# Performance work log

Hardware: AMD Instinct MI355X
Metric: run time of the kernel (lower is better)

The kernel has to match this reference:

```python
import jax, jax.numpy as jnp
import numpy as np

N = 100000      # nodes
E = 1600000     # edges (avg degree 16)
D_IN, D_H, D_OUT = 128, 128, 64
EPS = 1e-5      # BatchNorm1d eps


def setup_inputs() -> dict:
    key = jax.random.key(0)
    ks = jax.random.split(key, 8)
    x = jax.random.normal(ks[0], (N, D_IN), jnp.float32)
    edge_index = jax.random.randint(ks[1], (2, E), 0, N, dtype=jnp.int64)

    def glorot(k, i, o):
        return jax.random.normal(k, (i, o), jnp.float32) * np.float32(1.0 / np.sqrt(i))

    return {
        "x": x,
        "edge_index": edge_index,
        "W1": glorot(ks[2], D_IN, D_H), "b1": jnp.zeros((D_H,), jnp.float32),
        "g1": jnp.ones((D_H,), jnp.float32), "be1": jnp.zeros((D_H,), jnp.float32),
        "W2": glorot(ks[3], D_H, D_H), "b2": jnp.zeros((D_H,), jnp.float32),
        "g2": jnp.ones((D_H,), jnp.float32), "be2": jnp.zeros((D_H,), jnp.float32),
        "W3": glorot(ks[4], D_H, D_OUT), "b3": jnp.zeros((D_OUT,), jnp.float32),
    }


def gcn_conv(h, W, b, src, dst, norm_e, self_norm):
    # GCNConv: D^{-1/2}(A+I)D^{-1/2} h W + b  (self-loops handled analytically)
    hw = h @ W                                  # [N, out]
    msg = hw[src] * norm_e[:, None]             # [E, out] gather + scale
    agg = jax.ops.segment_sum(msg, dst, num_segments=N)
    return agg + hw * self_norm[:, None] + b


def batchnorm(x, g, b):
    mu = jnp.mean(x, axis=0)
    var = jnp.var(x, axis=0)
    return (x - mu) * jax.lax.rsqrt(var + EPS) * g + b


def reference(x, edge_index, W1, b1, g1, be1, W2, b2, g2, be2, W3, b3):
    src, dst = edge_index[0], edge_index[1]
    # degrees including self-loop
    deg = jax.ops.segment_sum(jnp.ones((E,), jnp.float32), dst, num_segments=N) + 1.0
    dis = jax.lax.rsqrt(deg)                    # deg^{-1/2}
    norm_e = dis[src] * dis[dst]                # per-edge norm
    self_norm = dis * dis                       # self-loop norm deg^{-1}

    h = jax.nn.relu(batchnorm(gcn_conv(x, W1, b1, src, dst, norm_e, self_norm), g1, be1))
    h = jax.nn.relu(batchnorm(gcn_conv(h, W2, b2, src, dst, norm_e, self_norm), g2, be2))
    return gcn_conv(h, W3, b3, src, dst, norm_e, self_norm)
```

## Files before the change

kernel.cpp:

```cpp
#include <hip/hip_runtime.h>
#include <hip/hip_bf16.h>

#define BN_EPS 1e-5f
#define BINSH 9
#define MAXNB 200
#define NBLK 256

typedef __attribute__((ext_vector_type(8))) short bf16x8v;
typedef __attribute__((ext_vector_type(4))) float f32x4v;

__device__ __forceinline__ float u2f(unsigned x) { return __uint_as_float(x); }
__device__ __forceinline__ unsigned short f2bf(float f) {
    union { __hip_bfloat16 h; unsigned short u; } cv;
    cv.h = __float2bfloat16(f);
    return cv.u;
}

__global__ void detect_kernel(const int* __restrict__ e32, int* __restrict__ flag) {
    if (threadIdx.x == 0 && blockIdx.x == 0) {
        int nz = 0;
        for (int i = 0; i < 64; ++i) nz += (e32[2*i + 1] != 0);
        *flag = (nz == 0) ? 1 : 0;
    }
}

__device__ __forceinline__ int edge_at(const void* p, long long i, int is64) {
    return is64 ? (int)((const long long*)p)[i] : ((const int*)p)[i];
}

__global__ __launch_bounds__(256) void histA_kernel(const void* __restrict__ eidx,
                                                    const int* __restrict__ flag,
                                                    int* __restrict__ hist2dT,
                                                    int* __restrict__ binhist,
                                                    int E, int NB, int per_block) {
    __shared__ int lh[MAXNB];
    const int t = threadIdx.x;
    for (int i = t; i < NB; i += 256) lh[i] = 0;
    __syncthreads();
    const int is64 = *flag;
    long long base = (long long)blockIdx.x * per_block;
    long long lim  = base + per_block;
    if (lim > E) lim = E;
    for (long long e = base + t; e < lim; e += 256) {
        int d = edge_at(eidx, (long long)E + e, is64);
        atomicAdd(&lh[d >> BINSH], 1);
    }
    __syncthreads();
    for (int i = t; i < NB; i += 256) {
        hist2dT[i * NBLK + blockIdx.x] = lh[i];
        atomicAdd(&binhist[i], lh[i]);
    }
}

__global__ void binscan_kernel(const int* __restrict__ binhist, int* __restrict__ binrp, int NB) {
    __shared__ int s[256];
    const int t = threadIdx.x;
    int v = (t < NB) ? binhist[t] : 0;
    s[t] = v;
    __syncthreads();
    for (int off = 1; off < 256; off <<= 1) {
        int x = (t >= off) ? s[t - off] : 0;
        __syncthreads();
        s[t] += x;
        __syncthreads();
    }
    if (t < NB) binrp[t] = s[t] - v;
    if (t == 0) binrp[NB] = s[255];
}

__global__ __launch_bounds__(256) void colscan_kernel(int* __restrict__ hist2dT,
                                                      const int* __restrict__ binrp) {
    __shared__ int s[256];
    const int b = blockIdx.x;
    const int t = threadIdx.x;
    int v = hist2dT[b * NBLK + t];
    s[t] = v;
    __syncthreads();
    for (int off = 1; off < 256; off <<= 1) {
        int x = (t >= off) ? s[t - off] : 0;
        __syncthreads();
        s[t] += x;
        __syncthreads();
    }
    hist2dT[b * NBLK + t] = binrp[b] + s[t] - v;
}

__global__ __launch_bounds__(256) void passB_kernel(const void* __restrict__ eidx,
                                                    const int* __restrict__ flag,
                                                    const int* __restrict__ hist2dT,
                                                    int2* __restrict__ ibuf,
                                                    int E, int NB, int per_block) {
    __shared__ int lbase[MAXNB];
    __shared__ int lcur[MAXNB];
    const int t = threadIdx.x;
    for (int i = t; i < NB; i += 256) {
        lbase[i] = hist2dT[i * NBLK + blockIdx.x];
        lcur[i]  = 0;
    }
    __syncthreads();
    const int is64 = *flag;
    long long base = (long long)blockIdx.x * per_block;
    long long lim  = base + per_block;
    if (lim > E) lim = E;
    for (long long e = base + t; e < lim; e += 256) {
        int sN = edge_at(eidx, e, is64);
        int d  = edge_at(eidx, (long long)E + e, is64);
        int b  = d >> BINSH;
        int pos = lbase[b] + atomicAdd(&lcur[b], 1);
        ibuf[pos] = make_int2(sN, d);
    }
}

__global__ __launch_bounds__(256) void binsort2_kernel(const int2* __restrict__ ibuf,
                                                       const int* __restrict__ binrp,
                                                       int* __restrict__ rp,
                                                       float* __restrict__ dis,
                                                       int2* __restrict__ ep, int N) {
    const int b  = blockIdx.x;
    const int d0 = b << BINSH;
    const int dc = min(1 << BINSH, N - d0);
    __shared__ int lcnt[1 << BINSH];
    __shared__ int lofs[1 << BINSH];
    __shared__ int s2[256];
    const int t = threadIdx.x;
    lcnt[t] = 0; lcnt[t + 256] = 0;
    __syncthreads();
    const int ib0 = binrp[b], ib1 = binrp[b + 1];
    const int nE  = ib1 - ib0;
    for (int i = t; i < nE; i += 256) {
        int2 sd = ibuf[ib0 + i];
        atomicAdd(&lcnt[sd.y - d0], 1);
    }
    __syncthreads();
    const int c0 = lcnt[2 * t], c1 = lcnt[2 * t + 1];
    const int pair = c0 + c1;
    s2[t] = pair;
    __syncthreads();
    for (int off = 1; off < 256; off <<= 1) {
        int x = (t >= off) ? s2[t - off] : 0;
        __syncthreads();
        s2[t] += x;
        __syncthreads();
    }
    const int pexcl = s2[t] - pair;
    if (2 * t < dc) {
        rp[d0 + 2 * t + 1] = ib0 + pexcl + c0;
        dis[d0 + 2 * t]    = rsqrtf((float)c0 + 1.0f);
    }
    if (2 * t + 1 < dc) {
        rp[d0 + 2 * t + 2] = ib0 + pexcl + pair;
        dis[d0 + 2 * t + 1] = rsqrtf((float)c1 + 1.0f);
    }
    if (b == 0 && t == 0) rp[0] = 0;
    lofs[2 * t]     = pexcl;
    lofs[2 * t + 1] = pexcl + c0;
    __syncthreads();
    for (int i = t; i < nE; i += 256) {
        int2 sd = ibuf[ib0 + i];
        int dl  = sd.y - d0;
        int pos = ib0 + atomicAdd(&lofs[dl], 1);
        ep[pos] = sd;
    }
}

__global__ void weight_kernel(int2* __restrict__ ep, const float* __restrict__ dis, int E) {
    int e = blockIdx.x * 256 + threadIdx.x;
    if (e >= E) return;
    int2 sd = ep[e];
    float w = dis[sd.x] * dis[sd.y];
    ep[e] = make_int2(sd.x, __float_as_int(w));
}

__global__ void prep_wt_kernel(const float* __restrict__ W, __hip_bfloat16* __restrict__ Wt,
                               int K, int DOUT) {
    int i = blockIdx.x * 256 + threadIdx.x;
    if (i < K * DOUT) {
        int k = i / DOUT, c = i % DOUT;
        Wt[c * K + k] = __float2bfloat16(W[i]);
    }
}

__device__ __forceinline__ void load8(const float* p, float* f) {
    float4 v0 = ((const float4*)p)[0];
    float4 v1 = ((const float4*)p)[1];
    f[0] = v0.x; f[1] = v0.y; f[2] = v0.z; f[3] = v0.w;
    f[4] = v1.x; f[5] = v1.y; f[6] = v1.z; f[7] = v1.w;
}
__device__ __forceinline__ void load8(const __hip_bfloat16* p, float* f) {
    uint4 v = *(const uint4*)p;
    f[0] = u2f(v.x << 16); f[1] = u2f(v.x & 0xffff0000u);
    f[2] = u2f(v.y << 16); f[3] = u2f(v.y & 0xffff0000u);
    f[4] = u2f(v.z << 16); f[5] = u2f(v.z & 0xffff0000u);
    f[6] = u2f(v.w << 16); f[7] = u2f(v.w & 0xffff0000u);
}

template <int DOUT, bool BN, typename TH>
__global__ __launch_bounds__(256) void mfma_gemm_kernel(const TH* __restrict__ H,
                                                        const __hip_bfloat16* __restrict__ Wt,
                                                        const float* __restrict__ bnst,
                                                        __hip_bfloat16* __restrict__ out, int N) {
    constexpr int NCT = DOUT / 16;
    constexpr int LDW = 136;
    __shared__ __hip_bfloat16 sWt[DOUT * LDW];
    const int t = threadIdx.x;
    for (int i = t; i < DOUT * 16; i += 256) {
        int row = i >> 4, seg = i & 15;
        *(uint4*)&sWt[row * LDW + seg * 8] = ((const uint4*)Wt)[i];
    }
    const int lane = t & 63, wid = t >> 6;
    const int kq = lane >> 4, mrow = lane & 15;
    const int grow = blockIdx.x * 64 + wid * 16 + mrow;
    const int lrow = min(grow, N - 1);
    bf16x8v afrag[4];
#pragma unroll
    for (int ks = 0; ks < 4; ++ks) {
        const int k0 = ks * 32 + kq * 8;
        float f[8];
        load8(H + (size_t)lrow * 128 + k0, f);
        if (BN) {
            float4 s0 = *(const float4*)(bnst + k0);
            float4 s1 = *(const float4*)(bnst + k0 + 4);
            float4 h0 = *(const float4*)(bnst + 128 + k0);
            float4 h1 = *(const float4*)(bnst + 128 + k0 + 4);
            f[0] = fmaxf(fmaf(f[0], s0.x, h0.x), 0.f);
            f[1] = fmaxf(fmaf(f[1], s0.y, h0.y), 0.f);
            f[2] = fmaxf(fmaf(f[2], s0.z, h0.z), 0.f);
            f[3] = fmaxf(fmaf(f[3], s0.w, h0.w), 0.f);
            f[4] = fmaxf(fmaf(f[4], s1.x, h1.x), 0.f);
            f[5] = fmaxf(fmaf(f[5], s1.y, h1.y), 0.f);
            f[6] = fmaxf(fmaf(f[6], s1.z, h1.z), 0.f);
            f[7] = fmaxf(fmaf(f[7], s1.w, h1.w), 0.f);
        }
        bf16x8v a;
#pragma unroll
        for (int j = 0; j < 8; ++j) a[j] = (short)f2bf(f[j]);
        afrag[ks] = a;
    }
    __syncthreads();
    f32x4v acc[NCT];
#pragma unroll
    for (int ct = 0; ct < NCT; ++ct) acc[ct] = (f32x4v){0.f, 0.f, 0.f, 0.f};
#pragma unroll
    for (int ct = 0; ct < NCT; ++ct) {
#pragma unroll
        for (int ks = 0; ks < 4; ++ks) {
            bf16x8v b = *(const bf16x8v*)&sWt[(ct * 16 + mrow) * LDW + ks * 32 + kq * 8];
            acc[ct] = __builtin_amdgcn_mfma_f32_16x16x32_bf16(afrag[ks], b, acc[ct], 0, 0, 0);
        }
    }
#pragma unroll
    for (int r = 0; r < 4; ++r) {
        int orow = blockIdx.x * 64 + wid * 16 + kq * 4 + r;
        if (orow < N) {
            __hip_bfloat16* op = out + (size_t)orow * DOUT + mrow;
#pragma unroll
            for (int ct = 0; ct < NCT; ++ct) {
                union { unsigned short u; __hip_bfloat16 h; } cv;
                cv.u = f2bf(acc[ct][r]);
                op[ct * 16] = cv.h;
            }
        }
    }
}

template <int D, bool OUTBF>
__global__ void agg_kernel(const __hip_bfloat16* __restrict__ hw, const int* __restrict__ rp,
                           const int2* __restrict__ ep, const float* __restrict__ dis,
                           const float* __restrict__ bias, void* __restrict__ outv, int N) {
    constexpr int LPR = D / 4;
    int gtid = blockIdx.x * blockDim.x + threadIdx.x;
    int n    = gtid / LPR;
    int lane = gtid % LPR;
    if (n >= N) return;
    const uint2* hw4 = (const uint2*)hw;
    float sn = dis[n];
    sn *= sn;
    uint2 hv = hw4[(size_t)n * LPR + lane];
    float a0 = u2f(hv.x << 16) * sn;
    float a1 = u2f(hv.x & 0xffff0000u) * sn;
    float a2 = u2f(hv.y << 16) * sn;
    float a3 = u2f(hv.y & 0xffff0000u) * sn;
    int e0 = rp[n], e1 = rp[n + 1];
    int e = e0;
    for (; e + 8 <= e1; e += 8) {
        int2 p[8];
        uint2 v[8];
#pragma unroll
        for (int j = 0; j < 8; ++j) p[j] = ep[e + j];
#pragma unroll
        for (int j = 0; j < 8; ++j) v[j] = hw4[(size_t)p[j].x * LPR + lane];
#pragma unroll
        for (int j = 0; j < 8; ++j) {
            float w = __int_as_float(p[j].y);
            a0 += u2f(v[j].x << 16) * w; a1 += u2f(v[j].x & 0xffff0000u) * w;
            a2 += u2f(v[j].y << 16) * w; a3 += u2f(v[j].y & 0xffff0000u) * w;
        }
    }
    for (; e + 4 <= e1; e += 4) {
        int2 p[4];
        uint2 v[4];
#pragma unroll
        for (int j = 0; j < 4; ++j) p[j] = ep[e + j];
#pragma unroll
        for (int j = 0; j < 4; ++j) v[j] = hw4[(size_t)p[j].x * LPR + lane];
#pragma unroll
        for (int j = 0; j < 4; ++j) {
            float w = __int_as_float(p[j].y);
            a0 += u2f(v[j].x << 16) * w; a1 += u2f(v[j].x & 0xffff0000u) * w;
            a2 += u2f(v[j].y << 16) * w; a3 += u2f(v[j].y & 0xffff0000u) * w;
        }
    }
    for (; e < e1; ++e) {
        int2 p = ep[e];
        uint2 v = hw4[(size_t)p.x * LPR + lane];
        float w = __int_as_float(p.y);
        a0 += u2f(v.x << 16) * w; a1 += u2f(v.x & 0xffff0000u) * w;
        a2 += u2f(v.y << 16) * w; a3 += u2f(v.y & 0xffff0000u) * w;
    }
    float4 bv = ((const float4*)bias)[lane];
    a0 += bv.x; a1 += bv.y; a2 += bv.z; a3 += bv.w;
    if (OUTBF) {
        ushort4 o;
        o.x = f2bf(a0); o.y = f2bf(a1); o.z = f2bf(a2); o.w = f2bf(a3);
        ((ushort4*)outv)[(size_t)n * LPR + lane] = o;
    } else {
        ((float4*)outv)[(size_t)n * LPR + lane] = make_float4(a0, a1, a2, a3);
    }
}

__global__ void bn_stats_kernel(const __hip_bfloat16* __restrict__ X, float* __restrict__ stats, int N) {
    const int t  = threadIdx.x;
    const int c4 = t & 31;
    const int rg = t >> 5;
    const uint2* X4 = (const uint2*)X;
    float s0=0,s1=0,s2=0,s3=0,q0=0,q1=0,q2=0,q3=0;
    for (int r = blockIdx.x * 8 + rg; r < N; r += gridDim.x * 8) {
        uint2 v = X4[(size_t)r * 32 + c4];
        float f0 = u2f(v.x << 16), f1 = u2f(v.x & 0xffff0000u);
        float f2 = u2f(v.y << 16), f3 = u2f(v.y & 0xffff0000u);
        s0 += f0; q0 += f0 * f0;
        s1 += f1; q1 += f1 * f1;
        s2 += f2; q2 += f2 * f2;
        s3 += f3; q3 += f3 * f3;
    }
    __shared__ float ls[8][32][8];
    ls[rg][c4][0] = s0; ls[rg][c4][1] = s1; ls[rg][c4][2] = s2; ls[rg][c4][3] = s3;
    ls[rg][c4][4] = q0; ls[rg][c4][5] = q1; ls[rg][c4][6] = q2; ls[rg][c4][7] = q3;
    __syncthreads();
    if (t < 32) {
        float a[8] = {0,0,0,0,0,0,0,0};
        for (int g = 0; g < 8; ++g)
            for (int k = 0; k < 8; ++k) a[k] += ls[g][t][k];
        for (int k = 0; k < 4; ++k) {
            atomicAdd(&stats[t * 4 + k], a[k]);
            atomicAdd(&stats[128 + t * 4 + k], a[4 + k]);
        }
    }
}

__global__ void bn_finalize_kernel(float* __restrict__ stats, const float* __restrict__ g,
                                   const float* __restrict__ be, float invN) {
    int c = threadIdx.x;
    if (c < 128) {
        float mu  = stats[c] * invN;
        float var = stats[c + 128] * invN - mu * mu;
        float sc  = g[c] * rsqrtf(var + BN_EPS);
        stats[c]       = sc;
        stats[c + 128] = be[c] - mu * sc;
    }
}

extern "C" void kernel_launch(void* const* d_in, const int* in_sizes, int n_in,
                              void* d_out, int out_size, void* d_ws, size_t ws_size,
                              hipStream_t stream) {
    const float* x   = (const float*)d_in[0];
    const void*  eix = d_in[1];
    const float* W1  = (const float*)d_in[2];
    const float* b1  = (const float*)d_in[3];
    const float* g1  = (const float*)d_in[4];
    const float* be1 = (const float*)d_in[5];
    const float* W2  = (const float*)d_in[6];
    const float* b2  = (const float*)d_in[7];
    const float* g2  = (const float*)d_in[8];
    const float* be2 = (const float*)d_in[9];
    const float* W3  = (const float*)d_in[10];
    const float* b3  = (const float*)d_in[11];
    float* outp = (float*)d_out;

    const int N = in_sizes[0] / 128;
    const int E = in_sizes[1] / 2;
    const int NB = (N + (1 << BINSH) - 1) >> BINSH;

    char* base = (char*)d_ws;
    size_t off = 0;
    auto alloc = [&](size_t bytes) -> char* {
        char* p = base + off;
        off = (off + bytes + 255) & ~(size_t)255;
        return p;
    };
    __hip_bfloat16* A = (__hip_bfloat16*)alloc((size_t)N * 128 * 2);
    __hip_bfloat16* B = (__hip_bfloat16*)alloc((size_t)N * 128 * 2);
    int*   rp      = (int*)alloc((size_t)(N + 1) * 4);
    float* dis     = (float*)alloc((size_t)N * 4);
    int2*  ep      = (int2*)alloc((size_t)E * 8);
    int2*  ibuf    = (int2*)alloc((size_t)E * 8);
    int*   hist2dT = (int*)alloc((size_t)MAXNB * NBLK * 4);
    int*   binhist = (int*)alloc(MAXNB * 4);
    int*   binrp   = (int*)alloc((MAXNB + 1) * 4);
    __hip_bfloat16* wt1 = (__hip_bfloat16*)alloc(128 * 128 * 2);
    __hip_bfloat16* wt2 = (__hip_bfloat16*)alloc(128 * 128 * 2);
    __hip_bfloat16* wt3 = (__hip_bfloat16*)alloc(64 * 128 * 2);
    float* stats1 = (float*)alloc(256 * 4);
    float* stats2 = (float*)alloc(256 * 4);
    int*   flag   = (int*)alloc(64);
    (void)ws_size; (void)n_in; (void)out_size;

    const int per_block = (E + NBLK - 1) / NBLK;

    detect_kernel<<<1, 64, 0, stream>>>((const int*)eix, flag);
    hipMemsetAsync(binhist, 0, MAXNB * 4, stream);
    histA_kernel<<<NBLK, 256, 0, stream>>>(eix, flag, hist2dT, binhist, E, NB, per_block);
    binscan_kernel<<<1, 256, 0, stream>>>(binhist, binrp, NB);
    colscan_kernel<<<NB, 256, 0, stream>>>(hist2dT, binrp);
    passB_kernel<<<NBLK, 256, 0, stream>>>(eix, flag, hist2dT, ibuf, E, NB, per_block);
    binsort2_kernel<<<NB, 256, 0, stream>>>(ibuf, binrp, rp, dis, ep, N);
    weight_kernel<<<(E + 255) / 256, 256, 0, stream>>>(ep, dis, E);

    prep_wt_kernel<<<64, 256, 0, stream>>>(W1, wt1, 128, 128);
    prep_wt_kernel<<<64, 256, 0, stream>>>(W2, wt2, 128, 128);
    prep_wt_kernel<<<32, 256, 0, stream>>>(W3, wt3, 128, 64);

    const float invN = 1.0f / (float)N;
    const int gemm_grid = (N + 63) / 64;
    const int agg128_grid  = (int)(((long long)N * 32 + 255) / 256);
    const int agg64_grid   = (int)(((long long)N * 16 + 255) / 256);

    mfma_gemm_kernel<128, false, float><<<gemm_grid, 256, 0, stream>>>(x, wt1, nullptr, A, N);
    agg_kernel<128, true><<<agg128_grid, 256, 0, stream>>>(A, rp, ep, dis, b1, B, N);
    hipMemsetAsync(stats1, 0, 256 * 4, stream);
    bn_stats_kernel<<<256, 256, 0, stream>>>(B, stats1, N);
    bn_finalize_kernel<<<1, 128, 0, stream>>>(stats1, g1, be1, invN);

    mfma_gemm_kernel<128, true, __hip_bfloat16><<<gemm_grid, 256, 0, stream>>>(B, wt2, stats1, A, N);
    agg_kernel<128, true><<<agg128_grid, 256, 0, stream>>>(A, rp, ep, dis, b2, B, N);
    hipMemsetAsync(stats2, 0, 256 * 4, stream);
    bn_stats_kernel<<<256, 256, 0, stream>>>(B, stats2, N);
    bn_finalize_kernel<<<1, 128, 0, stream>>>(stats2, g2, be2, invN);

    mfma_gemm_kernel<64, true, __hip_bfloat16><<<gemm_grid, 256, 0, stream>>>(B, wt3, stats2, A, N);
    agg_kernel<64, false><<<agg64_grid, 256, 0, stream>>>(A, rp, ep, dis, b3, outp, N);
}
```

Measured before the change: 375.9 us.

## Fuse BN stats into aggregation, finalize into GEMM, merge small setup kernels

Batch-norm sum and sum-of-squares are now accumulated inside the aggregation kernel through shared-memory then global atomics, and the finalize step is recomputed per block inside the next GEMM. This removes the separate stats and finalize kernels and their extra pass over the hidden activations. The aggregation also moves to 8 features per lane with 16-byte gathers and 4-way unrolling instead of 8-way. Detection of the edge-index width is folded into the histogram kernels, the three weight-prep launches become one, and the memsets are merged, which cuts launch count. In exchange the code adds shared-memory atomic contention in the aggregation and one atomic flush per block to global stats.

Result: slower. 613.5 us (+63.2%).

```diff
diff --git a/kernel.cpp b/kernel.cpp
--- a/kernel.cpp
+++ b/kernel.cpp
@@ -16,28 +16,31 @@
     return cv.u;
 }
 
-__global__ void detect_kernel(const int* __restrict__ e32, int* __restrict__ flag) {
-    if (threadIdx.x == 0 && blockIdx.x == 0) {
-        int nz = 0;
-        for (int i = 0; i < 64; ++i) nz += (e32[2*i + 1] != 0);
-        *flag = (nz == 0) ? 1 : 0;
-    }
-}
-
 __device__ __forceinline__ int edge_at(const void* p, long long i, int is64) {
     return is64 ? (int)((const long long*)p)[i] : ((const int*)p)[i];
 }
 
+__device__ __forceinline__ int detect_is64(const void* eidx, int* sflag, int t) {
+    if (t == 0) {
+        const int* e32 = (const int*)eidx;
+        int nz = 0;
+        for (int i = 0; i < 64; ++i) nz += (e32[2 * i + 1] != 0);
+        *sflag = (nz == 0) ? 1 : 0;
+    }
+    return 0;
+}
+
 __global__ __launch_bounds__(256) void histA_kernel(const void* __restrict__ eidx,
-                                                    const int* __restrict__ flag,
                                                     int* __restrict__ hist2dT,
                                                     int* __restrict__ binhist,
                                                     int E, int NB, int per_block) {
     __shared__ int lh[MAXNB];
-    const int t = threadIdx.x;
+    __shared__ int sflag;
+    const int t = threadIdx.x;
+    detect_is64(eidx, &sflag, t);
     for (int i = t; i < NB; i += 256) lh[i] = 0;
     __syncthreads();
-    const int is64 = *flag;
+    const int is64 = sflag;
     long long base = (long long)blockIdx.x * per_block;
     long long lim  = base + per_block;
     if (lim > E) lim = E;
@@ -86,19 +89,20 @@
 }
 
 __global__ __launch_bounds__(256) void passB_kernel(const void* __restrict__ eidx,
-                                                    const int* __restrict__ flag,
                                                     const int* __restrict__ hist2dT,
                                                     int2* __restrict__ ibuf,
                                                     int E, int NB, int per_block) {
     __shared__ int lbase[MAXNB];
     __shared__ int lcur[MAXNB];
-    const int t = threadIdx.x;
+    __shared__ int sflag;
+    const int t = threadIdx.x;
+    detect_is64(eidx, &sflag, t);
     for (int i = t; i < NB; i += 256) {
         lbase[i] = hist2dT[i * NBLK + blockIdx.x];
         lcur[i]  = 0;
     }
     __syncthreads();
-    const int is64 = *flag;
+    const int is64 = sflag;
     long long base = (long long)blockIdx.x * per_block;
     long long lim  = base + per_block;
     if (lim > E) lim = E;
@@ -171,12 +175,23 @@
     ep[e] = make_int2(sd.x, __float_as_int(w));
 }
 
-__global__ void prep_wt_kernel(const float* __restrict__ W, __hip_bfloat16* __restrict__ Wt,
-                               int K, int DOUT) {
+__global__ void prep_wt_all_kernel(const float* __restrict__ W1, const float* __restrict__ W2,
+                                   const float* __restrict__ W3,
+                                   __hip_bfloat16* __restrict__ wt1,
+                                   __hip_bfloat16* __restrict__ wt2,
+                                   __hip_bfloat16* __restrict__ wt3) {
     int i = blockIdx.x * 256 + threadIdx.x;
-    if (i < K * DOUT) {
-        int k = i / DOUT, c = i % DOUT;
-        Wt[c * K + k] = __float2bfloat16(W[i]);
+    if (i < 16384) {
+        int k = i >> 7, c = i & 127;
+        wt1[c * 128 + k] = __float2bfloat16(W1[i]);
+    } else if (i < 32768) {
+        int j = i - 16384;
+        int k = j >> 7, c = j & 127;
+        wt2[c * 128 + k] = __float2bfloat16(W2[j]);
+    } else if (i < 40960) {
+        int j = i - 32768;
+        int k = j >> 6, c = j & 63;
+        wt3[c * 128 + k] = __float2bfloat16(W3[j]);
     }
 }
 
@@ -197,16 +212,28 @@
 template <int DOUT, bool BN, typename TH>
 __global__ __launch_bounds__(256) void mfma_gemm_kernel(const TH* __restrict__ H,
                                                         const __hip_bfloat16* __restrict__ Wt,
-                                                        const float* __restrict__ bnst,
+                                                        const float* __restrict__ stats,
+                                                        const float* __restrict__ g,
+                                                        const float* __restrict__ be,
+                                                        float invN,
                                                         __hip_bfloat16* __restrict__ out, int N) {
     constexpr int NCT = DOUT / 16;
     constexpr int LDW = 136;
     __shared__ __hip_bfloat16 sWt[DOUT * LDW];
+    __shared__ float sBN[256];
     const int t = threadIdx.x;
     for (int i = t; i < DOUT * 16; i += 256) {
         int row = i >> 4, seg = i & 15;
         *(uint4*)&sWt[row * LDW + seg * 8] = ((const uint4*)Wt)[i];
     }
+    if (BN && t < 128) {
+        float mu  = stats[t] * invN;
+        float var = stats[128 + t] * invN - mu * mu;
+        float sc  = g[t] * rsqrtf(var + BN_EPS);
+        sBN[t]       = sc;
+        sBN[128 + t] = be[t] - mu * sc;
+    }
+    __syncthreads();
     const int lane = t & 63, wid = t >> 6;
     const int kq = lane >> 4, mrow = lane & 15;
     const int grow = blockIdx.x * 64 + wid * 16 + mrow;
@@ -218,10 +245,10 @@
         float f[8];
         load8(H + (size_t)lrow * 128 + k0, f);
         if (BN) {
-            float4 s0 = *(const float4*)(bnst + k0);
-            float4 s1 = *(const float4*)(bnst + k0 + 4);
-            float4 h0 = *(const float4*)(bnst + 128 + k0);
-            float4 h1 = *(const float4*)(bnst + 128 + k0 + 4);
+            float4 s0 = *(const float4*)&sBN[k0];
+            float4 s1 = *(const float4*)&sBN[k0 + 4];
+            float4 h0 = *(const float4*)&sBN[128 + k0];
+            float4 h1 = *(const float4*)&sBN[128 + k0 + 4];
             f[0] = fmaxf(fmaf(f[0], s0.x, h0.x), 0.f);
             f[1] = fmaxf(fmaf(f[1], s0.y, h0.y), 0.f);
             f[2] = fmaxf(fmaf(f[2], s0.z, h0.z), 0.f);
@@ -236,7 +263,6 @@
         for (int j = 0; j < 8; ++j) a[j] = (short)f2bf(f[j]);
         afrag[ks] = a;
     }
-    __syncthreads();
     f32x4v acc[NCT];
 #pragma unroll
     for (int ct = 0; ct < NCT; ++ct) acc[ct] = (f32x4v){0.f, 0.f, 0.f, 0.f};
@@ -263,110 +289,93 @@
     }
 }
 
-template <int D, bool OUTBF>
-__global__ void agg_kernel(const __hip_bfloat16* __restrict__ hw, const int* __restrict__ rp,
-                           const int2* __restrict__ ep, const float* __restrict__ dis,
-                           const float* __restrict__ bias, void* __restrict__ outv, int N) {
-    constexpr int LPR = D / 4;
-    int gtid = blockIdx.x * blockDim.x + threadIdx.x;
-    int n    = gtid / LPR;
-    int lane = gtid % LPR;
-    if (n >= N) return;
-    const uint2* hw4 = (const uint2*)hw;
-    float sn = dis[n];
-    sn *= sn;
-    uint2 hv = hw4[(size_t)n * LPR + lane];
-    float a0 = u2f(hv.x << 16) * sn;
-    float a1 = u2f(hv.x & 0xffff0000u) * sn;
-    float a2 = u2f(hv.y << 16) * sn;
-    float a3 = u2f(hv.y & 0xffff0000u) * sn;
-    int e0 = rp[n], e1 = rp[n + 1];
-    int e = e0;
-    for (; e + 8 <= e1; e += 8) {
-        int2 p[8];
-        uint2 v[8];
-#pragma unroll
-        for (int j = 0; j < 8; ++j) p[j] = ep[e + j];
-#pragma unroll
-        for (int j = 0; j < 8; ++j) v[j] = hw4[(size_t)p[j].x * LPR + lane];
-#pragma unroll
-        for (int j = 0; j < 8; ++j) {
-            float w = __int_as_float(p[j].y);
-            a0 += u2f(v[j].x << 16) * w; a1 += u2f(v[j].x & 0xffff0000u) * w;
-            a2 += u2f(v[j].y << 16) * w; a3 += u2f(v[j].y & 0xffff0000u) * w;
-        }
-    }
-    for (; e + 4 <= e1; e += 4) {
-        int2 p[4];
-        uint2 v[4];
-#pragma unroll
-        for (int j = 0; j < 4; ++j) p[j] = ep[e + j];
-#pragma unroll
-        for (int j = 0; j < 4; ++j) v[j] = hw4[(size_t)p[j].x * LPR + lane];
-#pragma unroll
-        for (int j = 0; j < 4; ++j) {
-            float w = __int_as_float(p[j].y);
-            a0 += u2f(v[j].x << 16) * w; a1 += u2f(v[j].x & 0xffff0000u) * w;
-            a2 += u2f(v[j].y << 16) * w; a3 += u2f(v[j].y & 0xffff0000u) * w;
-        }
-    }
-    for (; e < e1; ++e) {
-        int2 p = ep[e];
-        uint2 v = hw4[(size_t)p.x * LPR + lane];
-        float w = __int_as_float(p.y);
-        a0 += u2f(v.x << 16) * w; a1 += u2f(v.x & 0xffff0000u) * w;
-        a2 += u2f(v.y << 16) * w; a3 += u2f(v.y & 0xffff0000u) * w;
-    }
-    float4 bv = ((const float4*)bias)[lane];
-    a0 += bv.x; a1 += bv.y; a2 += bv.z; a3 += bv.w;
-    if (OUTBF) {
-        ushort4 o;
-        o.x = f2bf(a0); o.y = f2bf(a1); o.z = f2bf(a2); o.w = f2bf(a3);
-        ((ushort4*)outv)[(size_t)n * LPR + lane] = o;
-    } else {
-        ((float4*)outv)[(size_t)n * LPR + lane] = make_float4(a0, a1, a2, a3);
-    }
-}
-
-__global__ void bn_stats_kernel(const __hip_bfloat16* __restrict__ X, float* __restrict__ stats, int N) {
-    const int t  = threadIdx.x;
-    const int c4 = t & 31;
-    const int rg = t >> 5;
-    const uint2* X4 = (const uint2*)X;
-    float s0=0,s1=0,s2=0,s3=0,q0=0,q1=0,q2=0,q3=0;
-    for (int r = blockIdx.x * 8 + rg; r < N; r += gridDim.x * 8) {
-        uint2 v = X4[(size_t)r * 32 + c4];
-        float f0 = u2f(v.x << 16), f1 = u2f(v.x & 0xffff0000u);
-        float f2 = u2f(v.y << 16), f3 = u2f(v.y & 0xffff0000u);
-        s0 += f0; q0 += f0 * f0;
-        s1 += f1; q1 += f1 * f1;
-        s2 += f2; q2 += f2 * f2;
-        s3 += f3; q3 += f3 * f3;
-    }
-    __shared__ float ls[8][32][8];
-    ls[rg][c4][0] = s0; ls[rg][c4][1] = s1; ls[rg][c4][2] = s2; ls[rg][c4][3] = s3;
-    ls[rg][c4][4] = q0; ls[rg][c4][5] = q1; ls[rg][c4][6] = q2; ls[rg][c4][7] = q3;
-    __syncthreads();
-    if (t < 32) {
-        float a[8] = {0,0,0,0,0,0,0,0};
-        for (int g = 0; g < 8; ++g)
-            for (int k = 0; k < 8; ++k) a[k] += ls[g][t][k];
-        for (int k = 0; k < 4; ++k) {
-            atomicAdd(&stats[t * 4 + k], a[k]);
-            atomicAdd(&stats[128 + t * 4 + k], a[4 + k]);
-        }
-    }
-}
-
-__global__ void bn_finalize_kernel(float* __restrict__ stats, const float* __restrict__ g,
-                                   const float* __restrict__ be, float invN) {
-    int c = threadIdx.x;
-    if (c < 128) {
-        float mu  = stats[c] * invN;
-        float var = stats[c + 128] * invN - mu * mu;
-        float sc  = g[c] * rsqrtf(var + BN_EPS);
-        stats[c]       = sc;
-        stats[c + 128] = be[c] - mu * sc;
+__device__ __forceinline__ void acc8(float* a, uint4 v, float w) {
+    a[0] += u2f(v.x << 16) * w;  a[1] += u2f(v.x & 0xffff0000u) * w;
+    a[2] += u2f(v.y << 16) * w;  a[3] += u2f(v.y & 0xffff0000u) * w;
+    a[4] += u2f(v.z << 16) * w;  a[5] += u2f(v.z & 0xffff0000u) * w;
+    a[6] += u2f(v.w << 16) * w;  a[7] += u2f(v.w & 0xffff0000u) * w;
+}
+
+template <int D, bool OUTBF, bool STATS>
+__global__ __launch_bounds__(256) void agg_kernel(const __hip_bfloat16* __restrict__ hw,
+                                                  const int* __restrict__ rp,
+                                                  const int2* __restrict__ ep,
+                                                  const float* __restrict__ dis,
+                                                  const float* __restrict__ bias,
+                                                  void* __restrict__ outv,
+                                                  float* __restrict__ stats, int N) {
+    constexpr int LPR = D / 8;
+    __shared__ float ssum[128];
+    __shared__ float ssq[128];
+    const int t = threadIdx.x;
+    if (STATS) {
+        if (t < 128) { ssum[t] = 0.f; ssq[t] = 0.f; }
+        __syncthreads();
+    }
+    const int gtid = blockIdx.x * 256 + t;
+    const int n    = gtid / LPR;
+    const int lane = gtid % LPR;
+    const bool valid = (n < N);
+    const uint4* hw8 = (const uint4*)hw;
+    float a[8] = {0.f, 0.f, 0.f, 0.f, 0.f, 0.f, 0.f, 0.f};
+    if (valid) {
+        float sn = dis[n];
+        sn *= sn;
+        uint4 hv = hw8[(size_t)n * LPR + lane];
+        acc8(a, hv, sn);
+        int e0 = rp[n], e1 = rp[n + 1];
+        int e = e0;
+        for (; e + 4 <= e1; e += 4) {
+            int2 p0 = ep[e + 0];
+            int2 p1 = ep[e + 1];
+            int2 p2 = ep[e + 2];
+            int2 p3 = ep[e + 3];
+            uint4 v0 = hw8[(size_t)p0.x * LPR + lane];
+            uint4 v1 = hw8[(size_t)p1.x * LPR + lane];
+            uint4 v2 = hw8[(size_t)p2.x * LPR + lane];
+            uint4 v3 = hw8[(size_t)p3.x * LPR + lane];
+            acc8(a, v0, __int_as_float(p0.y));
+            acc8(a, v1, __int_as_float(p1.y));
+            acc8(a, v2, __int_as_float(p2.y));
+            acc8(a, v3, __int_as_float(p3.y));
+        }
+        for (; e < e1; ++e) {
+            int2 p = ep[e];
+            uint4 v = hw8[(size_t)p.x * LPR + lane];
+            acc8(a, v, __int_as_float(p.y));
+        }
+        float4 b0 = *(const float4*)(bias + lane * 8);
+        float4 b1 = *(const float4*)(bias + lane * 8 + 4);
+        a[0] += b0.x; a[1] += b0.y; a[2] += b0.z; a[3] += b0.w;
+        a[4] += b1.x; a[5] += b1.y; a[6] += b1.z; a[7] += b1.w;
+    }
+    if (STATS) {
+        if (valid) {
+#pragma unroll
+            for (int j = 0; j < 8; ++j) {
+                atomicAdd(&ssum[lane * 8 + j], a[j]);
+                atomicAdd(&ssq[lane * 8 + j], a[j] * a[j]);
+            }
+        }
+        __syncthreads();
+        if (t < 128) {
+            atomicAdd(&stats[t], ssum[t]);
+            atomicAdd(&stats[128 + t], ssq[t]);
+        }
+    }
+    if (valid) {
+        if (OUTBF) {
+            uint4 o;
+            o.x = (unsigned)f2bf(a[0]) | ((unsigned)f2bf(a[1]) << 16);
+            o.y = (unsigned)f2bf(a[2]) | ((unsigned)f2bf(a[3]) << 16);
+            o.z = (unsigned)f2bf(a[4]) | ((unsigned)f2bf(a[5]) << 16);
+            o.w = (unsigned)f2bf(a[6]) | ((unsigned)f2bf(a[7]) << 16);
+            ((uint4*)outv)[(size_t)n * LPR + lane] = o;
+        } else {
+            float4* op = (float4*)outv + ((size_t)n * D + lane * 8) / 4;
+            op[0] = make_float4(a[0], a[1], a[2], a[3]);
+            op[1] = make_float4(a[4], a[5], a[6], a[7]);
+        }
     }
 }
 
@@ -405,48 +414,43 @@
     int2*  ep      = (int2*)alloc((size_t)E * 8);
     int2*  ibuf    = (int2*)alloc((size_t)E * 8);
     int*   hist2dT = (int*)alloc((size_t)MAXNB * NBLK * 4);
+    int*   binrp   = (int*)alloc((MAXNB + 1) * 4);
     int*   binhist = (int*)alloc(MAXNB * 4);
-    int*   binrp   = (int*)alloc((MAXNB + 1) * 4);
+    float* stats1  = (float*)alloc(256 * 4);
+    float* stats2  = (float*)alloc(256 * 4);
     __hip_bfloat16* wt1 = (__hip_bfloat16*)alloc(128 * 128 * 2);
     __hip_bfloat16* wt2 = (__hip_bfloat16*)alloc(128 * 128 * 2);
     __hip_bfloat16* wt3 = (__hip_bfloat16*)alloc(64 * 128 * 2);
-    float* stats1 = (float*)alloc(256 * 4);
-    float* stats2 = (float*)alloc(256 * 4);
-    int*   flag   = (int*)alloc(64);
     (void)ws_size; (void)n_in; (void)out_size;
 
     const int per_block = (E + NBLK - 1) / NBLK;
 
-    detect_kernel<<<1, 64, 0, stream>>>((const int*)eix, flag);
-    hipMemsetAsync(binhist, 0, MAXNB * 4, stream);
-    histA_kernel<<<NBLK, 256, 0, stream>>>(eix, flag, hist2dT, binhist, E, NB, per_block);
+    hipMemsetAsync(binhist, 0, 3 * 1024, stream);
+    histA_kernel<<<NBLK, 256, 0, stream>>>(eix, hist2dT, binhist, E, NB, per_block);
     binscan_kernel<<<1, 256, 0, stream>>>(binhist, binrp, NB);
     colscan_kernel<<<NB, 256, 0, stream>>>(hist2dT, binrp);
-    passB_kernel<<<NBLK, 256, 0, stream>>>(eix, flag, hist2dT, ibuf, E, NB, per_block);
+    passB_kernel<<<NBLK, 256, 0, stream>>>(eix, hist2dT, ibuf, E, NB, per_block);
     binsort2_kernel<<<NB, 256, 0, stream>>>(ibuf, binrp, rp, dis, ep, N);
     weight_kernel<<<(E + 255) / 256, 256, 0, stream>>>(ep, dis, E);
-
-    prep_wt_kernel<<<64, 256, 0, stream>>>(W1, wt1, 128, 128);
-    prep_wt_kernel<<<64, 256, 0, stream>>>(W2, wt2, 128, 128);
-    prep_wt_kernel<<<32, 256, 0, stream>>>(W3, wt3, 128, 64);
+    prep_wt_all_kernel<<<160, 256, 0, stream>>>(W1, W2, W3, wt1, wt2, wt3);
 
     const float invN = 1.0f / (float)N;
-    const int gemm_grid = (N + 63) / 64;
-    const int agg128_grid  = (int)(((long long)N * 32 + 255) / 256);
-    const int agg64_grid   = (int)(((long long)N * 16 + 255) / 256);
-
-    mfma_gemm_kernel<128, false, float><<<gemm_grid, 256, 0, stream>>>(x, wt1, nullptr, A, N);
-    agg_kernel<128, true><<<agg128_grid, 256, 0, stream>>>(A, rp, ep, dis, b1, B, N);
-    hipMemsetAsync(stats1, 0, 256 * 4, stream);
-    bn_stats_kernel<<<256, 256, 0, stream>>>(B, stats1, N);
-    bn_finalize_kernel<<<1, 128, 0, stream>>>(stats1, g1, be1, invN);
-
-    mfma_gemm_kernel<128, true, __hip_bfloat16><<<gemm_grid, 256, 0, stream>>>(B, wt2, stats1, A, N);
-    agg_kernel<128, true><<<agg128_grid, 256, 0, stream>>>(A, rp, ep, dis, b2, B, N);
-    hipMemsetAsync(stats2, 0, 256 * 4, stream);
-    bn_stats_kernel<<<256, 256, 0, stream>>>(B, stats2, N);
-    bn_finalize_kernel<<<1, 128, 0, stream>>>(stats2, g2, be2, invN);
-
-    mfma_gemm_kernel<64, true, __hip_bfloat16><<<gemm_grid, 256, 0, stream>>>(B, wt3, stats2, A, N);
-    agg_kernel<64, false><<<agg64_grid, 256, 0, stream>>>(A, rp, ep, dis, b3, outp, N);
-}
+    const int gemm_grid   = (N + 63) / 64;
+    const int agg128_grid = (int)(((long long)N * 16 + 255) / 256);
+    const int agg64_grid  = (int)(((long long)N * 8 + 255) / 256);
+
+    mfma_gemm_kernel<128, false, float><<<gemm_grid, 256, 0, stream>>>(
+        x, wt1, nullptr, nullptr, nullptr, 0.f, A, N);
+    agg_kernel<128, true, true><<<agg128_grid, 256, 0, stream>>>(
+        A, rp, ep, dis, b1, B, stats1, N);
+
+    mfma_gemm_kernel<128, true, __hip_bfloat16><<<gemm_grid, 256, 0, stream>>>(
+        B, wt2, stats1, g1, be1, invN, A, N);
+    agg_kernel<128, true, true><<<agg128_grid, 256, 0, stream>>>(
+        A, rp, ep, dis, b2, B, stats2, N);
+
+    mfma_gemm_kernel<64, true, __hip_bfloat16><<<gemm_grid, 256, 0, stream>>>(
+        B, wt3, stats2, g2, be2, invN, A, N);
+    agg_kernel<64, false, false><<<agg64_grid, 256, 0, stream>>>(
+        A, rp, ep, dis, b3, outp, nullptr, N);
+}
```
